# Optimization experiments

Hardware: AMD Instinct MI355X
Metric: run time of the kernel (lower is better)

Reference implementation:

```python
import jax, jax.numpy as jnp
import numpy as np

N = 8192          # number of prototypes
D = 128           # proto_dim == hidden_dim (residual requires equality)
H = 2             # GAT heads
K = 3             # k_neighbors + 1 (k_neighbors=2 hard-coded in forward)
NEG_SLOPE = 0.2   # PyG GATConv default leaky relu slope
LN_EPS = 1e-5


def setup_inputs() -> dict:
    key = jax.random.key(0)
    ks = jax.random.split(key, 6)
    prototypes = jax.random.normal(ks[0], (N, D), dtype=jnp.float32)
    labels = jax.random.randint(ks[1], (N,), 0, 1024, dtype=jnp.int64)
    # GATConv params: lin maps D -> H*D (concat=False => per-head dim = hidden_dim)
    W = jax.random.normal(ks[2], (D, H * D), dtype=jnp.float32) / np.sqrt(D)
    att_src = jax.random.normal(ks[3], (H, D), dtype=jnp.float32) / np.sqrt(D)
    att_dst = jax.random.normal(ks[4], (H, D), dtype=jnp.float32) / np.sqrt(D)
    bias = jnp.zeros((D,), dtype=jnp.float32)
    gamma = jnp.ones((D,), dtype=jnp.float32)   # LayerNorm weight
    beta = jnp.zeros((D,), dtype=jnp.float32)   # LayerNorm bias
    return {"prototypes": prototypes, "labels": labels, "W": W,
            "att_src": att_src, "att_dst": att_dst, "bias": bias,
            "gamma": gamma, "beta": beta}


def _knn_edges(x):
    # Squared euclidean distances (same ordering as torch.cdist -> same topk indices).
    sq = jnp.sum(x * x, axis=-1)
    d2 = sq[:, None] + sq[None, :] - 2.0 * (x @ x.T)          # [N, N]
    _, idx = jax.lax.top_k(-d2, K)                            # [N, K] smallest dists
    # topk includes self (dist 0); module masks self-edges then GATConv re-adds
    # self loops, so the effective edge set is exactly the topk set -> static E=N*K.
    src = jnp.repeat(jnp.arange(x.shape[0]), K)               # edge source j
    dst = idx.reshape(-1)                                     # edge target i
    return src, dst


def _gat(x, src, dst, W, att_src, att_dst, bias):
    n = x.shape[0]
    xp = (x @ W).reshape(n, H, D)                             # [N, H, C]
    a_s = jnp.sum(xp * att_src[None], axis=-1)                # [N, H]
    a_d = jnp.sum(xp * att_dst[None], axis=-1)                # [N, H]
    e = a_s[src] + a_d[dst]                                   # [E, H]
    e = jax.nn.leaky_relu(e, NEG_SLOPE)
    # segment softmax over incoming edges of each destination node
    m = jax.ops.segment_max(e, dst, num_segments=n)           # [N, H]
    w = jnp.exp(e - m[dst])
    denom = jax.ops.segment_sum(w, dst, num_segments=n)       # [N, H]
    alpha = w / denom[dst]                                    # [E, H]
    msg = alpha[:, :, None] * xp[src]                         # [E, H, C]
    out = jax.ops.segment_sum(msg, dst, num_segments=n)       # [N, H, C]
    return out.mean(axis=1) + bias                            # concat=False -> head mean


def reference(prototypes, labels, W, att_src, att_dst, bias, gamma, beta):
    x = prototypes
    src, dst = _knn_edges(x)
    x_new = _gat(x, src, dst, W, att_src, att_dst, bias)
    mu = jnp.mean(x_new, axis=-1, keepdims=True)
    var = jnp.var(x_new, axis=-1, keepdims=True)
    x_new = (x_new - mu) * jax.lax.rsqrt(var + LN_EPS) * gamma + beta
    x_new = jax.nn.relu(x_new)
    # dropout layers are identity in eval mode
    return x + x_new
```

## Files before the change

kernel.cpp:

```cpp
#include <hip/hip_runtime.h>
#include <hip/hip_bf16.h>
#include <math.h>

#define GN 8192
#define GD 128
#define GH 2
#define GK 3
#define NEG_SLOPE 0.2f
#define LN_EPS 1e-5f

using short8  = __attribute__((ext_vector_type(8)))  short;
using float16 = __attribute__((ext_vector_type(16))) float;
using f32x4   = __attribute__((ext_vector_type(4)))  float;

__device__ __forceinline__ float wred(float v) {
    #pragma unroll
    for (int o = 32; o > 0; o >>= 1) v += __shfl_xor(v, o, 64);
    return v;
}

__device__ __forceinline__ unsigned fenc(float f) {
    unsigned b = __float_as_uint(f);
    return (b & 0x80000000u) ? ~b : (b | 0x80000000u);
}

__device__ __forceinline__ float rawbf2f(unsigned short s) {
    return __uint_as_float(((unsigned)s) << 16);
}
__device__ __forceinline__ unsigned short f2rawbf(float f) {
    __hip_bfloat16 b = __float2bfloat16(f);
    unsigned short r; __builtin_memcpy(&r, &b, 2);
    return r;
}
__device__ __forceinline__ unsigned umin2(unsigned a, unsigned b) { return a < b ? a : b; }
__device__ __forceinline__ unsigned umax2(unsigned a, unsigned b) { return a > b ? a : b; }

__global__ void k_pre(const float* __restrict__ W, const float* __restrict__ att_src,
                      const float* __restrict__ att_dst,
                      unsigned short* __restrict__ Wth, unsigned short* __restrict__ Wtl,
                      float* __restrict__ uvec) {
    __shared__ float vs[128];
    int b = blockIdx.x, t = threadIdx.x;
    if (b < 128) {
        int e = b * 256 + t;
        int d = e >> 8, j = e & 255;
        int h = j >> 7, c = j & 127;
        int k = h * 128 + d;
        float w = W[e];
        unsigned short hi = f2rawbf(w);
        Wth[c * 256 + k] = hi;
        Wtl[c * 256 + k] = f2rawbf(w - rawbf2f(hi));
    } else {
        int bb = b - 128;
        int h = bb & 1;
        const float* v = (bb < 2 ? att_src : att_dst) + h * 128;
        if (t < 128) vs[t] = v[t];
        __syncthreads();
        int d = t >> 1, half = t & 1;
        const float* wr = W + (size_t)d * 256 + h * 128 + half * 64;
        float s = 0.f;
        for (int c = 0; c < 64; c++) s += wr[c] * vs[half * 64 + c];
        s += __shfl_xor(s, 1, 64);
        if (half == 0) uvec[bb * 128 + d] = s;
    }
}

__global__ void k_conv(const float* __restrict__ x, const float* __restrict__ uvec,
                       float* __restrict__ sq,
                       unsigned short* __restrict__ xa, unsigned short* __restrict__ xb,
                       float* __restrict__ a_s, float* __restrict__ a_d,
                       int* __restrict__ cnt, int* __restrict__ curs) {
    int row = blockIdx.x * 4 + (threadIdx.x >> 6);
    int lane = threadIdx.x & 63;
    const float* xr = x + (size_t)row * GD;
    float a0 = xr[lane], a1 = xr[lane + 64];
    float s = wred(a0 * a0 + a1 * a1);
    unsigned short* ar = xa + (size_t)row * 144;
    unsigned short* br = xb + (size_t)row * 144;
    ar[lane] = f2rawbf(-2.f * a0); ar[lane + 64] = f2rawbf(-2.f * a1);
    br[lane] = f2rawbf(a0);        br[lane + 64] = f2rawbf(a1);
    float s0 = wred(a0 * uvec[lane]       + a1 * uvec[64 + lane]);
    float s1 = wred(a0 * uvec[128 + lane] + a1 * uvec[192 + lane]);
    float d0 = wred(a0 * uvec[256 + lane] + a1 * uvec[320 + lane]);
    float d1 = wred(a0 * uvec[384 + lane] + a1 * uvec[448 + lane]);
    if (lane < 16) {
        unsigned short av = 0, bv = 0;
        if (lane == 0)      { av = f2rawbf(s + 512.f); bv = 0x3F80; }
        else if (lane == 1) { float hi = rawbf2f(f2rawbf(s + 512.f));
                              av = f2rawbf(s + 512.f - hi); bv = 0x3F80; }
        ar[128 + lane] = av; br[128 + lane] = bv;
        if (lane == 0) {
            sq[row] = s;
            a_s[row * 2] = s0; a_s[row * 2 + 1] = s1;
            a_d[row * 2] = d0; a_d[row * 2 + 1] = d1;
            cnt[row] = 0; curs[row] = 0;
        }
    }
}

#define INS(U0,U1,U2,U3,kk) do {                                   \
    unsigned m0_ = umax2(U0,(kk)); U0 = umin2(U0,(kk));            \
    unsigned m1_ = umax2(U1,m0_);  U1 = umin2(U1,m0_);             \
    unsigned m2_ = umax2(U2,m1_);  U2 = umin2(U2,m1_);             \
    U3 = umin2(U3,m2_); } while(0)

#define TOPK16(A, U0,U1,U2,U3, rbase) do {                                        \
    _Pragma("unroll")                                                             \
    for (int q4_ = 0; q4_ < 4; q4_++) {                                           \
        unsigned c0_ = __float_as_uint((A)[q4_ * 4 + 0]);                         \
        unsigned c1_ = __float_as_uint((A)[q4_ * 4 + 1]);                         \
        unsigned c2_ = __float_as_uint((A)[q4_ * 4 + 2]);                         \
        unsigned c3_ = __float_as_uint((A)[q4_ * 4 + 3]);                         \
        unsigned qm_ = umin2(umin2(c0_, c1_), umin2(c2_, c3_));                   \
        if ((qm_ & 0xFFFFE000u) <= U3) {                                          \
            INS(U0,U1,U2,U3, (c0_ & 0xFFFFE000u) | (unsigned)((rbase) + 0 + 8 * q4_)); \
            INS(U0,U1,U2,U3, (c1_ & 0xFFFFE000u) | (unsigned)((rbase) + 1 + 8 * q4_)); \
            INS(U0,U1,U2,U3, (c2_ & 0xFFFFE000u) | (unsigned)((rbase) + 2 + 8 * q4_)); \
            INS(U0,U1,U2,U3, (c3_ & 0xFFFFE000u) | (unsigned)((rbase) + 3 + 8 * q4_)); \
        }                                                                         \
    } } while(0)

#define STAGE_HALF(buf, rowbase)                                                  \
    do {                                                                          \
        _Pragma("unroll")                                                         \
        for (int s_ = 0; s_ < 3; s_++) {                                          \
            if (s_ < 2 || t < 64) {                                               \
                int q_ = s_ * 256 + t;           \
                int kb_ = q_ >> 5, r_ = q_ & 31;                                  \
                __builtin_amdgcn_global_load_lds(                                 \
                    (const __attribute__((address_space(1))) unsigned*)           \
                        (xa + (size_t)((rowbase) + r_) * 144 + kb_ * 8),          \
                    (__attribute__((address_space(3))) unsigned*)&At[(buf)][q_ * 8],\
                    16, 0, 0);                                                    \
            }                                                                     \
        }                                                                         \
    } while (0)

__launch_bounds__(256, 6)
__global__ void k_gemm_topk(const unsigned short* __restrict__ xa,
                            const unsigned short* __restrict__ xb,
                            unsigned* __restrict__ cand) {
    __shared__ __align__(16) unsigned short At[2][18 * 32 * 8];
    int t = threadIdx.x;
    int w = t >> 6, lane = t & 63, h = lane >> 5, n = lane & 31;
    int col = blockIdx.x * 128 + w * 32 + n;
    int sb = blockIdx.y;
    int rb0 = sb * 256;

    short8 bfrag[9];
    #pragma unroll
    for (int kc = 0; kc < 9; kc++)
        bfrag[kc] = *(const short8*)(xb + (size_t)col * 144 + (2 * kc + h) * 8);

    STAGE_HALF(0, rb0);
    asm volatile("s_waitcnt vmcnt(0)" ::: "memory");
    __builtin_amdgcn_s_barrier();

    unsigned T0 = 0xFFFFFFFFu, T1 = 0xFFFFFFFFu, T2 = 0xFFFFFFFFu, T3 = 0xFFFFFFFFu;

    #pragma unroll 1
    for (int ht = 0; ht < 8; ht++) {
        int cur = ht & 1;
        if (ht < 7) STAGE_HALF(cur ^ 1, rb0 + (ht + 1) * 32);

        float16 acc = (float16)(0.f);

        #pragma unroll
        for (int kc = 0; kc < 9; kc++) {
            short8 a = *(const short8*)&At[cur][(((2 * kc + h) * 32) + n) * 8];
            acc = __builtin_amdgcn_mfma_f32_32x32x16_bf16(a, bfrag[kc], acc, 0, 0, 0);
        }

        int rbq = rb0 + ht * 32 + 4 * h;
        TOPK16(acc, T0, T1, T2, T3, rbq);

        if (ht < 7) {
            asm volatile("s_waitcnt vmcnt(0)" ::: "memory");
            __builtin_amdgcn_s_barrier();
        }
    }

    unsigned p0 = (unsigned)__shfl_xor((int)T0, 32), p1 = (unsigned)__shfl_xor((int)T1, 32),
             p2 = (unsigned)__shfl_xor((int)T2, 32), p3 = (unsigned)__shfl_xor((int)T3, 32);
    INS(T0,T1,T2,T3, p0); INS(T0,T1,T2,T3, p1);
    INS(T0,T1,T2,T3, p2); INS(T0,T1,T2,T3, p3);
    if (h == 0) {
        uint4 o = make_uint4(T0, T1, T2, T3);
        *(uint4*)(cand + (size_t)col * 128 + sb * 4) = o;
    }
}

__device__ __forceinline__ int clampN(int v) {
    return v < 0 ? 0 : (v >= GN ? GN - 1 : v);
}

__global__ void k_refine(const unsigned* __restrict__ cand,
                         const float* __restrict__ x, const float* __restrict__ sq,
                         int* __restrict__ fidx, int* __restrict__ cnt) {
    int t = threadIdx.x, wv = t >> 6, lane = t & 63;
    int j = blockIdx.x * 4 + wv;
    int c = lane >> 2, g = lane & 3;

    unsigned k0 = cand[(size_t)j * 128 + lane];
    unsigned k1 = cand[(size_t)j * 128 + 64 + lane];
    int myidx = 0;
    #pragma unroll
    for (int r = 0; r < 16; r++) {
        unsigned m = umin2(k0, k1);
        #pragma unroll
        for (int o = 32; o > 0; o >>= 1)
            m = umin2(m, (unsigned)__shfl_xor((int)m, o, 64));
        myidx = (c == r) ? (int)(m & 8191u) : myidx;
        k0 = (k0 == m) ? 0xFFFFFFFFu : k0;
        k1 = (k1 == m) ? 0xFFFFFFFFu : k1;
    }

    const float* xi = x + (size_t)myidx * GD + g * 32;
    const float* xj = x + (size_t)j * GD + g * 32;
    float p = 0.f;
    #pragma unroll
    for (int d4 = 0; d4 < 8; d4++) {
        float4 a = *(const float4*)(xi + d4 * 4);
        float4 b = *(const float4*)(xj + d4 * 4);
        p += a.x * b.x + a.y * b.y + a.z * b.z + a.w * b.w;
    }
    p += __shfl_xor(p, 1, 64);
    p += __shfl_xor(p, 2, 64);
    float d2 = sq[j] + sq[myidx] - 2.f * p;
    unsigned long long key = ((unsigned long long)fenc(d2) << 32) | (unsigned)myidx;

    int out3[3];
    #pragma unroll
    for (int r = 0; r < 3; r++) {
        unsigned long long k = key;
        #pragma unroll
        for (int o = 4; o <= 32; o <<= 1) {
            unsigned long long other = __shfl_xor(k, o, 64);
            k = k < other ? k : other;
        }
        out3[r] = (int)(unsigned)(k & 8191u);
        key = (key == k) ? ~0ull : key;
    }
    if (lane == 0) {
        int i0 = clampN(out3[0]), i1 = clampN(out3[1]), i2 = clampN(out3[2]);
        fidx[j * 3 + 0] = i0; fidx[j * 3 + 1] = i1; fidx[j * 3 + 2] = i2;
        atomicAdd(&cnt[i0], 1); atomicAdd(&cnt[i1], 1); atomicAdd(&cnt[i2], 1);
    }
}

__global__ void k_scan(const int* __restrict__ cnt, int* __restrict__ offs) {
    __shared__ __align__(16) int buf[8192];
    __shared__ int wtot[4];
    int t = threadIdx.x, wv = t >> 6, lane = t & 63;
    #pragma unroll
    for (int j = 0; j < 8; j++)
        ((int4*)buf)[j * 256 + t] = ((const int4*)cnt)[j * 256 + t];
    __syncthreads();
    int loc[32], s = 0;
    #pragma unroll
    for (int k = 0; k < 32; k++) { loc[k] = s; s += buf[t * 32 + k]; }
    int inc = s;
    #pragma unroll
    for (int d = 1; d < 64; d <<= 1) {
        int nv = __shfl_up(inc, d, 64);
        if (lane >= d) inc += nv;
    }
    if (lane == 63) wtot[wv] = inc;
    __syncthreads();
    int wbase = 0;
    #pragma unroll
    for (int wq = 0; wq < 4; wq++) wbase += (wq < wv) ? wtot[wq] : 0;
    int base = wbase + inc - s;
    #pragma unroll
    for (int k = 0; k < 32; k++) buf[t * 32 + k] = base + loc[k];
    __syncthreads();
    #pragma unroll
    for (int j = 0; j < 8; j++)
        ((int4*)offs)[j * 256 + t] = ((int4*)buf)[j * 256 + t];
    if (t == 255) offs[GN] = wtot[0] + wtot[1] + wtot[2] + wtot[3];
}

__global__ void k_fill(const int* __restrict__ fidx, const int* __restrict__ offs,
                       int* __restrict__ cursor, int* __restrict__ elist,
                       const float* __restrict__ a_s, const float* __restrict__ a_d,
                       float2* __restrict__ ew) {
    int eid = blockIdx.x * 256 + threadIdx.x;
    int i = clampN(fidx[eid]);
    int src = eid / 3;
    float2 as = ((const float2*)a_s)[src];
    float2 ad = ((const float2*)a_d)[i];
    float e0 = as.x + ad.x; e0 = e0 >= 0.f ? e0 : NEG_SLOPE * e0;
    float e1 = as.y + ad.y; e1 = e1 >= 0.f ? e1 : NEG_SLOPE * e1;
    float w0 = expf(e0), w1 = expf(e1);
    int pos = atomicAdd(&cursor[i], 1);
    int slot = offs[i] + pos;
    if (slot < GN * GK) { elist[slot] = src; ew[slot] = make_float2(w0, w1); }
}

__launch_bounds__(512, 4)
__global__ void k_out(const int* __restrict__ offs, const int* __restrict__ elst,
                      const float2* __restrict__ ew,
                      const float* __restrict__ x,
                      const unsigned short* __restrict__ Wth,
                      const unsigned short* __restrict__ Wtl,
                      const float* __restrict__ bias, const float* __restrict__ gamma,
                      const float* __restrict__ beta, float* __restrict__ out) {
    __shared__ unsigned short zh[16][264];
    __shared__ unsigned short zl[16][264];
    __shared__ float os[16][132];
    int t = threadIdx.x, i0 = blockIdx.x * 16;
    int wv = t >> 6, lane = t & 63;
    int eslot = lane >> 3, g = lane & 7;

    #pragma unroll
    for (int pp = 0; pp < 2; pp++) {
        int r = wv * 2 + pp, node = i0 + r;
        int s = offs[node], e = offs[node + 1];
        float acc0[16], acc1[16];
        #pragma unroll
        for (int q = 0; q < 16; q++) { acc0[q] = 0.f; acc1[q] = 0.f; }
        float w0s = 0.f, w1s = 0.f;
        for (int k0 = s; k0 < e; k0 += 8) {
            int k = k0 + eslot;
            bool valid = k < e;
            int j = valid ? elst[k] : 0;
            float2 wv2 = valid ? ew[k] : make_float2(0.f, 0.f);
            const float* xr = x + (size_t)j * GD + g * 16;
            float4 x0 = *(const float4*)(xr);
            float4 x1 = *(const float4*)(xr + 4);
            float4 x2 = *(const float4*)(xr + 8);
            float4 x3 = *(const float4*)(xr + 12);
            float xv[16] = {x0.x, x0.y, x0.z, x0.w, x1.x, x1.y, x1.z, x1.w,
                            x2.x, x2.y, x2.z, x2.w, x3.x, x3.y, x3.z, x3.w};
            #pragma unroll
            for (int q = 0; q < 16; q++) {
                acc0[q] += wv2.x * xv[q];
                acc1[q] += wv2.y * xv[q];
            }
            w0s += wv2.x; w1s += wv2.y;
        }
        #pragma unroll
        for (int m = 8; m <= 32; m <<= 1) {
            #pragma unroll
            for (int q = 0; q < 16; q++) {
                acc0[q] += __shfl_xor(acc0[q], m, 64);
                acc1[q] += __shfl_xor(acc1[q], m, 64);
            }
            w0s += __shfl_xor(w0s, m, 64);
            w1s += __shfl_xor(w1s, m, 64);
        }
        if (lane < 8) {
            float dn0 = 0.5f / w0s, dn1 = 0.5f / w1s;
            #pragma unroll
            for (int q = 0; q < 16; q += 2) {
                float a0 = acc0[q] * dn0, a1 = acc0[q + 1] * dn0;
                unsigned short h0 = f2rawbf(a0), h1 = f2rawbf(a1);
                *(unsigned*)&zh[r][lane * 16 + q] = (unsigned)h0 | ((unsigned)h1 << 16);
                *(unsigned*)&zl[r][lane * 16 + q] =
                    (unsigned)f2rawbf(a0 - rawbf2f(h0)) |
                    ((unsigned)f2rawbf(a1 - rawbf2f(h1)) << 16);
                float b0 = acc1[q] * dn1, b1 = acc1[q + 1] * dn1;
                unsigned short p0 = f2rawbf(b0), p1 = f2rawbf(b1);
                *(unsigned*)&zh[r][128 + lane * 16 + q] = (unsigned)p0 | ((unsigned)p1 << 16);
                *(unsigned*)&zl[r][128 + lane * 16 + q] =
                    (unsigned)f2rawbf(b0 - rawbf2f(p0)) |
                    ((unsigned)f2rawbf(b1 - rawbf2f(p1)) << 16);
            }
        }
    }
    __syncthreads();

    {
        int qd = lane >> 4, an = lane & 15;
        int c = wv * 16 + an;
        f32x4 acc = {0.f, 0.f, 0.f, 0.f};
        #pragma unroll
        for (int s = 0; s < 8; s++) {
            int ko = s * 32 + qd * 8;
            short8 ah = *(const short8*)&zh[an][ko];
            short8 al = *(const short8*)&zl[an][ko];
            short8 bh = *(const short8*)(Wth + (size_t)c * 256 + ko);
            short8 bl = *(const short8*)(Wtl + (size_t)c * 256 + ko);
            acc = __builtin_amdgcn_mfma_f32_16x16x32_bf16(ah, bh, acc, 0, 0, 0);
            acc = __builtin_amdgcn_mfma_f32_16x16x32_bf16(al, bh, acc, 0, 0, 0);
            acc = __builtin_amdgcn_mfma_f32_16x16x32_bf16(ah, bl, acc, 0, 0, 0);
        }
        #pragma unroll
        for (int r = 0; r < 4; r++) os[qd * 4 + r][c] = acc[r];
    }
    __syncthreads();

    #pragma unroll
    for (int pp = 0; pp < 2; pp++) {
        int r = wv * 2 + pp, node = i0 + r;
        float y0 = os[r][lane] + bias[lane];
        float y1 = os[r][lane + 64] + bias[lane + 64];
        float mu = wred(y0 + y1) * (1.f / 128.f);
        float c0 = y0 - mu, c1 = y1 - mu;
        float var = wred(c0 * c0 + c1 * c1) * (1.f / 128.f);
        float rs2 = 1.f / sqrtf(var + LN_EPS);
        float n0 = c0 * rs2 * gamma[lane] + beta[lane];
        float n1 = c1 * rs2 * gamma[lane + 64] + beta[lane + 64];
        n0 = n0 > 0.f ? n0 : 0.f;
        n1 = n1 > 0.f ? n1 : 0.f;
        out[(size_t)node * GD + lane]      = x[(size_t)node * GD + lane] + n0;
        out[(size_t)node * GD + lane + 64] = x[(size_t)node * GD + lane + 64] + n1;
    }
}

extern "C" void kernel_launch(void* const* d_in, const int* in_sizes, int n_in,
                              void* d_out, int out_size, void* d_ws, size_t ws_size,
                              hipStream_t stream) {
    const float* x       = (const float*)d_in[0];
    const float* W       = (const float*)d_in[2];
    const float* att_src = (const float*)d_in[3];
    const float* att_dst = (const float*)d_in[4];
    const float* bias    = (const float*)d_in[5];
    const float* gamma   = (const float*)d_in[6];
    const float* beta    = (const float*)d_in[7];
    float* out = (float*)d_out;

    char* w = (char*)d_ws;
    unsigned short* xa = (unsigned short*)w; w += (size_t)GN * 144 * 2;
    unsigned short* xb = (unsigned short*)w; w += (size_t)GN * 144 * 2;
    unsigned* cand = (unsigned*)w;           w += (size_t)GN * 128 * 4;
    float2* ew  = (float2*)w; w += (size_t)GN * GK * 8;
    unsigned short* Wth = (unsigned short*)w; w += (size_t)256 * 128 * 2;
    unsigned short* Wtl = (unsigned short*)w; w += (size_t)256 * 128 * 2;
    float* uvec = (float*)w; w += (size_t)4 * 128 * 4;
    float* sq   = (float*)w; w += (size_t)GN * 4;
    float* a_s  = (float*)w; w += (size_t)GN * GH * 4;
    float* a_d  = (float*)w; w += (size_t)GN * GH * 4;
    int*   fidx = (int*)w;   w += (size_t)GN * GK * 4;
    int*   cnt  = (int*)w;   w += (size_t)GN * 4;
    int*   curs = (int*)w;   w += (size_t)GN * 4;
    int*   offs = (int*)w;   w += (size_t)(GN + 1) * 4;
    int*   elst = (int*)w;   w += (size_t)GN * GK * 4;
    size_t need = (size_t)((char*)w - (char*)d_ws);
    if (ws_size < need) return;

    k_pre<<<132, 256, 0, stream>>>(W, att_src, att_dst, Wth, Wtl, uvec);
    k_conv<<<GN / 4, 256, 0, stream>>>(x, uvec, sq, xa, xb, a_s, a_d, cnt, curs);
    k_gemm_topk<<<dim3(64, 32), 256, 0, stream>>>(xa, xb, cand);
    k_refine<<<GN / 4, 256, 0, stream>>>(cand, x, sq, fidx, cnt);
    k_scan<<<1, 256, 0, stream>>>(cnt, offs);
    k_fill<<<GN * GK / 256, 256, 0, stream>>>(fidx, offs, curs, elst, a_s, a_d, ew);
    k_out<<<GN / 16, 512, 0, stream>>>(offs, elst, ew, x, Wth, Wtl, bias, gamma, beta, out);
}
```

Baseline: 166.7 us.

## Merge prep kernels and fold scan into fill to cut launches

```diff
diff --git a/kernel.cpp b/kernel.cpp
--- a/kernel.cpp
+++ b/kernel.cpp
@@ -35,10 +35,12 @@
 __device__ __forceinline__ unsigned umin2(unsigned a, unsigned b) { return a < b ? a : b; }
 __device__ __forceinline__ unsigned umax2(unsigned a, unsigned b) { return a > b ? a : b; }
 
-__global__ void k_pre(const float* __restrict__ W, const float* __restrict__ att_src,
-                      const float* __restrict__ att_dst,
-                      unsigned short* __restrict__ Wth, unsigned short* __restrict__ Wtl,
-                      float* __restrict__ uvec) {
+__global__ void k_prep(const float* __restrict__ W, const float* __restrict__ att_src,
+                       const float* __restrict__ att_dst, const float* __restrict__ x,
+                       unsigned short* __restrict__ Wth, unsigned short* __restrict__ Wtl,
+                       float* __restrict__ uvec, float* __restrict__ sq,
+                       unsigned short* __restrict__ xa, unsigned short* __restrict__ xb,
+                       int* __restrict__ cnt, int* __restrict__ curs) {
     __shared__ float vs[128];
     int b = blockIdx.x, t = threadIdx.x;
     if (b < 128) {
@@ -50,7 +52,7 @@
         unsigned short hi = f2rawbf(w);
         Wth[c * 256 + k] = hi;
         Wtl[c * 256 + k] = f2rawbf(w - rawbf2f(hi));
-    } else {
+    } else if (b < 132) {
         int bb = b - 128;
         int h = bb & 1;
         const float* v = (bb < 2 ? att_src : att_dst) + h * 128;
@@ -62,38 +64,26 @@
         for (int c = 0; c < 64; c++) s += wr[c] * vs[half * 64 + c];
         s += __shfl_xor(s, 1, 64);
         if (half == 0) uvec[bb * 128 + d] = s;
-    }
-}
-
-__global__ void k_conv(const float* __restrict__ x, const float* __restrict__ uvec,
-                       float* __restrict__ sq,
-                       unsigned short* __restrict__ xa, unsigned short* __restrict__ xb,
-                       float* __restrict__ a_s, float* __restrict__ a_d,
-                       int* __restrict__ cnt, int* __restrict__ curs) {
-    int row = blockIdx.x * 4 + (threadIdx.x >> 6);
-    int lane = threadIdx.x & 63;
-    const float* xr = x + (size_t)row * GD;
-    float a0 = xr[lane], a1 = xr[lane + 64];
-    float s = wred(a0 * a0 + a1 * a1);
-    unsigned short* ar = xa + (size_t)row * 144;
-    unsigned short* br = xb + (size_t)row * 144;
-    ar[lane] = f2rawbf(-2.f * a0); ar[lane + 64] = f2rawbf(-2.f * a1);
-    br[lane] = f2rawbf(a0);        br[lane + 64] = f2rawbf(a1);
-    float s0 = wred(a0 * uvec[lane]       + a1 * uvec[64 + lane]);
-    float s1 = wred(a0 * uvec[128 + lane] + a1 * uvec[192 + lane]);
-    float d0 = wred(a0 * uvec[256 + lane] + a1 * uvec[320 + lane]);
-    float d1 = wred(a0 * uvec[384 + lane] + a1 * uvec[448 + lane]);
-    if (lane < 16) {
-        unsigned short av = 0, bv = 0;
-        if (lane == 0)      { av = f2rawbf(s + 512.f); bv = 0x3F80; }
-        else if (lane == 1) { float hi = rawbf2f(f2rawbf(s + 512.f));
-                              av = f2rawbf(s + 512.f - hi); bv = 0x3F80; }
-        ar[128 + lane] = av; br[128 + lane] = bv;
-        if (lane == 0) {
-            sq[row] = s;
-            a_s[row * 2] = s0; a_s[row * 2 + 1] = s1;
-            a_d[row * 2] = d0; a_d[row * 2 + 1] = d1;
-            cnt[row] = 0; curs[row] = 0;
+    } else {
+        int row = (b - 132) * 4 + (t >> 6);
+        int lane = t & 63;
+        const float* xr = x + (size_t)row * GD;
+        float a0 = xr[lane], a1 = xr[lane + 64];
+        float s = wred(a0 * a0 + a1 * a1);
+        unsigned short* ar = xa + (size_t)row * 144;
+        unsigned short* br = xb + (size_t)row * 144;
+        ar[lane] = f2rawbf(-2.f * a0); ar[lane + 64] = f2rawbf(-2.f * a1);
+        br[lane] = f2rawbf(a0);        br[lane + 64] = f2rawbf(a1);
+        if (lane < 16) {
+            unsigned short av = 0, bv = 0;
+            if (lane == 0)      { av = f2rawbf(s + 512.f); bv = 0x3F80; }
+            else if (lane == 1) { float hi = rawbf2f(f2rawbf(s + 512.f));
+                                  av = f2rawbf(s + 512.f - hi); bv = 0x3F80; }
+            ar[128 + lane] = av; br[128 + lane] = bv;
+            if (lane == 0) {
+                sq[row] = s;
+                cnt[row] = 0; curs[row] = 0;
+            }
         }
     }
 }
@@ -196,8 +186,26 @@
 
 __global__ void k_refine(const unsigned* __restrict__ cand,
                          const float* __restrict__ x, const float* __restrict__ sq,
-                         int* __restrict__ fidx, int* __restrict__ cnt) {
+                         const float* __restrict__ uvec,
+                         int* __restrict__ fidx, int* __restrict__ cnt,
+                         float* __restrict__ a_s, float* __restrict__ a_d) {
     int t = threadIdx.x, wv = t >> 6, lane = t & 63;
+
+    if (blockIdx.x >= 2048) {
+        int row = (blockIdx.x - 2048) * 4 + wv;
+        const float* xr = x + (size_t)row * GD;
+        float a0 = xr[lane], a1 = xr[lane + 64];
+        float s0 = wred(a0 * uvec[lane]       + a1 * uvec[64 + lane]);
+        float s1 = wred(a0 * uvec[128 + lane] + a1 * uvec[192 + lane]);
+        float d0 = wred(a0 * uvec[256 + lane] + a1 * uvec[320 + lane]);
+        float d1 = wred(a0 * uvec[384 + lane] + a1 * uvec[448 + lane]);
+        if (lane == 0) {
+            a_s[row * 2] = s0; a_s[row * 2 + 1] = s1;
+            a_d[row * 2] = d0; a_d[row * 2 + 1] = d1;
+        }
+        return;
+    }
+
     int j = blockIdx.x * 4 + wv;
     int c = lane >> 2, g = lane & 3;
 
@@ -248,10 +256,15 @@
     }
 }
 
-__global__ void k_scan(const int* __restrict__ cnt, int* __restrict__ offs) {
+__global__ void k_fill(const int* __restrict__ cnt, int* __restrict__ offs,
+                       const int* __restrict__ fidx,
+                       int* __restrict__ cursor, int* __restrict__ elist,
+                       const float* __restrict__ a_s, const float* __restrict__ a_d,
+                       float2* __restrict__ ew) {
     __shared__ __align__(16) int buf[8192];
     __shared__ int wtot[4];
     int t = threadIdx.x, wv = t >> 6, lane = t & 63;
+
     #pragma unroll
     for (int j = 0; j < 8; j++)
         ((int4*)buf)[j * 256 + t] = ((const int4*)cnt)[j * 256 + t];
@@ -274,17 +287,14 @@
     #pragma unroll
     for (int k = 0; k < 32; k++) buf[t * 32 + k] = base + loc[k];
     __syncthreads();
-    #pragma unroll
-    for (int j = 0; j < 8; j++)
-        ((int4*)offs)[j * 256 + t] = ((int4*)buf)[j * 256 + t];
-    if (t == 255) offs[GN] = wtot[0] + wtot[1] + wtot[2] + wtot[3];
-}
-
-__global__ void k_fill(const int* __restrict__ fidx, const int* __restrict__ offs,
-                       int* __restrict__ cursor, int* __restrict__ elist,
-                       const float* __restrict__ a_s, const float* __restrict__ a_d,
-                       float2* __restrict__ ew) {
-    int eid = blockIdx.x * 256 + threadIdx.x;
+    if (blockIdx.x == 0) {
+        #pragma unroll
+        for (int j = 0; j < 8; j++)
+            ((int4*)offs)[j * 256 + t] = ((int4*)buf)[j * 256 + t];
+        if (t == 255) offs[GN] = wtot[0] + wtot[1] + wtot[2] + wtot[3];
+    }
+
+    int eid = blockIdx.x * 256 + t;
     int i = clampN(fidx[eid]);
     int src = eid / 3;
     float2 as = ((const float2*)a_s)[src];
@@ -293,7 +303,7 @@
     float e1 = as.y + ad.y; e1 = e1 >= 0.f ? e1 : NEG_SLOPE * e1;
     float w0 = expf(e0), w1 = expf(e1);
     int pos = atomicAdd(&cursor[i], 1);
-    int slot = offs[i] + pos;
+    int slot = buf[i] + pos;
     if (slot < GN * GK) { elist[slot] = src; ew[slot] = make_float2(w0, w1); }
 }
 
@@ -439,11 +449,10 @@
     size_t need = (size_t)((char*)w - (char*)d_ws);
     if (ws_size < need) return;
 
-    k_pre<<<132, 256, 0, stream>>>(W, att_src, att_dst, Wth, Wtl, uvec);
-    k_conv<<<GN / 4, 256, 0, stream>>>(x, uvec, sq, xa, xb, a_s, a_d, cnt, curs);
+    k_prep<<<132 + GN / 4, 256, 0, stream>>>(W, att_src, att_dst, x, Wth, Wtl,
+                                             uvec, sq, xa, xb, cnt, curs);
     k_gemm_topk<<<dim3(64, 32), 256, 0, stream>>>(xa, xb, cand);
-    k_refine<<<GN / 4, 256, 0, stream>>>(cand, x, sq, fidx, cnt);
-    k_scan<<<1, 256, 0, stream>>>(cnt, offs);
-    k_fill<<<GN * GK / 256, 256, 0, stream>>>(fidx, offs, curs, elst, a_s, a_d, ew);
+    k_refine<<<GN / 4 + GN / 4, 256, 0, stream>>>(cand, x, sq, uvec, fidx, cnt, a_s, a_d);
+    k_fill<<<GN * GK / 256, 256, 0, stream>>>(cnt, offs, fidx, curs, elst, a_s, a_d, ew);
     k_out<<<GN / 16, 512, 0, stream>>>(offs, elst, ew, x, Wth, Wtl, bias, gamma, beta, out);
 }
```

Measured after the change: 159.6 us, median of 2. 1.04x faster.
